# Kernel tuning notes

Hardware: AMD Instinct MI355X
Metric: run time of the kernel (lower is better)

The kernel has to match this reference:

```python
import jax, jax.numpy as jnp
import numpy as np
from jax import lax

B, D, K = 65536, 256, 32  # batch, num_latent_dims, flow_depth


def setup_inputs() -> dict:
    key = jax.random.key(0)
    k1, k2, k3, k4, k5 = jax.random.split(key, 5)
    X = jax.random.normal(k1, (B, D), dtype=jnp.float32)
    h = jax.random.normal(k2, (B, D), dtype=jnp.float32)  # passed through, unused by planar math
    u = jax.random.normal(k3, (K, D), dtype=jnp.float32) * 0.1
    w = jax.random.normal(k4, (K, D), dtype=jnp.float32) * 0.1
    b = jax.random.normal(k5, (K,), dtype=jnp.float32) * 0.1
    return {"X": X, "h": h, "u": u, "w": w, "b": b}


def _planar_chain(z0, u, w, b):
    """Sequential planar normalizing flow: z_{k+1} = z_k + u_hat_k * tanh(w_k.z_k + b_k)."""

    def step(z, params):
        u_k, w_k, b_k = params  # (D,), (D,), scalar
        # enforce invertibility: u_hat so that w.u_hat >= -1
        wu = jnp.dot(w_k, u_k)
        u_hat = u_k + (jax.nn.softplus(wu) - 1.0 - wu) * w_k / jnp.dot(w_k, w_k)
        lin = z @ w_k + b_k              # (B,)
        t = jnp.tanh(lin)                # (B,)
        z_new = z + t[:, None] * u_hat[None, :]
        # psi = (1 - t^2) w ; log|det J| = log|1 + psi.u_hat|
        log_det = jnp.log(jnp.abs(1.0 + (1.0 - t * t) * jnp.dot(w_k, u_hat)) + 1e-8)
        return z_new, log_det

    z_final, log_dets = lax.scan(step, z0, (u, w, b))
    return z_final, log_dets  # (B, D), (K, B)


def reference(X, h, u, w, b):
    z = X.reshape(X.shape[0], X.shape[1])  # view(B, D, -1) then view(B, D) -> (B, D)
    z_final, log_det_jacobians = _planar_chain(z, u, w, b)
    return z_final, log_det_jacobians
```

## Files before the change

kernel.cpp:

```cpp
#include <hip/hip_runtime.h>


typedef __attribute__((ext_vector_type(8))) short short8;
typedef __attribute__((ext_vector_type(4))) float f32x4;

#define B_ 65536
#define D_ 256
#define ROWS 64
#define NTHR 512
#define GRID (B_ / ROWS)

#define WSB_WH 0
#define WSB_WL 16896
#define WSB_UTH 33792
#define WSB_UTL 54272
#define WSB_G 74752
#define WSB_C 78848

#define WH_H 0
#define WL_H 8448
#define UH_H 0
#define UL_H 10240
#define XH_H 20480
#define XL_H 23040
#define LDS_HALVES 25600
#define P_STR 65

__device__ __forceinline__ void bfsplit(float x, unsigned short& h, unsigned short& l) {
  unsigned xb = __float_as_uint(x) & 0xffff0000u;
  h = (unsigned short)(xb >> 16);
  float r = x - __uint_as_float(xb);
  l = (unsigned short)(__float_as_uint(r) >> 16);
}

__global__ __launch_bounds__(256) void nf_gen(const float* __restrict__ u_in,
                                              const float* __restrict__ w_in,
                                              float* __restrict__ ws) {
  __shared__ float wTg[8192];
  __shared__ float ug[8192];
  __shared__ float wu_s[32], ww_s[32], coefs_s[32];
  const int t = threadIdx.x;
  {
    const int k = t & 31, d0 = (t >> 5) * 32;
    const float4* wp = (const float4*)(w_in + k * 256 + d0);
#pragma unroll
    for (int q = 0; q < 8; ++q) {
      float4 v = wp[q];
      wTg[(d0 + q * 4 + 0) * 32 + k] = v.x;
      wTg[(d0 + q * 4 + 1) * 32 + k] = v.y;
      wTg[(d0 + q * 4 + 2) * 32 + k] = v.z;
      wTg[(d0 + q * 4 + 3) * 32 + k] = v.w;
    }
#pragma unroll
    for (int q = 0; q < 8; ++q)
      ((float4*)ug)[t + 256 * q] = ((const float4*)u_in)[t + 256 * q];
  }
  __syncthreads();
  const int k = t & 31, jg = t >> 5;
  float m1[4] = {0.f, 0.f, 0.f, 0.f}, m2[4] = {0.f, 0.f, 0.f, 0.f};
#pragma unroll 4
  for (int dc = 0; dc < 64; ++dc) {
    float wk[4];
    float4 wj[4], uj[4];
#pragma unroll
    for (int i = 0; i < 4; ++i) wk[i] = wTg[(dc * 4 + i) * 32 + k];
#pragma unroll
    for (int i = 0; i < 4; ++i) wj[i] = *(const float4*)&wTg[(dc * 4 + i) * 32 + jg * 4];
#pragma unroll
    for (int i = 0; i < 4; ++i) uj[i] = *(const float4*)&ug[(jg * 4 + i) * 256 + dc * 4];
#pragma unroll
    for (int i = 0; i < 4; ++i) {
      m1[i] = fmaf(uj[i].x, wk[0], m1[i]);
      m1[i] = fmaf(uj[i].y, wk[1], m1[i]);
      m1[i] = fmaf(uj[i].z, wk[2], m1[i]);
      m1[i] = fmaf(uj[i].w, wk[3], m1[i]);
    }
    const float* w0 = (const float*)&wj[0];
    const float* w1 = (const float*)&wj[1];
    const float* w2 = (const float*)&wj[2];
    const float* w3 = (const float*)&wj[3];
#pragma unroll
    for (int i = 0; i < 4; ++i) {
      m2[i] = fmaf(w0[i], wk[0], m2[i]);
      m2[i] = fmaf(w1[i], wk[1], m2[i]);
      m2[i] = fmaf(w2[i], wk[2], m2[i]);
      m2[i] = fmaf(w3[i], wk[3], m2[i]);
    }
  }
  if ((k >> 2) == jg) {
    wu_s[k] = m1[k & 3];
    ww_s[k] = m2[k & 3];
  }
  __syncthreads();
  if (t < 32) {
    float wu = wu_s[t], ww = ww_s[t];
    float sp = fmaxf(wu, 0.f) + log1pf(__expf(-fabsf(wu)));
    coefs_s[t] = (sp - 1.f - wu) / ww;
    ((float*)((char*)ws + WSB_C))[t] = sp - 1.f;
  }
  __syncthreads();
  {
    float* gws = (float*)((char*)ws + WSB_G);
#pragma unroll
    for (int i = 0; i < 4; ++i)
      gws[k * 32 + jg * 4 + i] = fmaf(coefs_s[jg * 4 + i], m2[i], m1[i]);
  }
  {
    const int k2 = t >> 3, d0 = (t & 7) * 32;
    const float ck = coefs_s[k2];
    unsigned short* whp = (unsigned short*)((char*)ws + WSB_WH);
    unsigned short* wlp = (unsigned short*)((char*)ws + WSB_WL);
    unsigned short* uthp = (unsigned short*)((char*)ws + WSB_UTH);
    unsigned short* utlp = (unsigned short*)((char*)ws + WSB_UTL);
    const float4* wp2 = (const float4*)(w_in + k2 * 256 + d0);
    const float4* up2 = (const float4*)(u_in + k2 * 256 + d0);
#pragma unroll
    for (int q = 0; q < 8; ++q) {
      float4 wv = wp2[q], uv = up2[q];
      const float wf[4] = {wv.x, wv.y, wv.z, wv.w};
      const float uf[4] = {uv.x, uv.y, uv.z, uv.w};
#pragma unroll
      for (int i = 0; i < 4; ++i) {
        unsigned short hh, ll;
        bfsplit(wf[i], hh, ll);
        whp[k2 * 264 + d0 + q * 4 + i] = hh;
        wlp[k2 * 264 + d0 + q * 4 + i] = ll;
        float uhv = fmaf(ck, wf[i], uf[i]);
        bfsplit(uhv, hh, ll);
        uthp[(d0 + q * 4 + i) * 40 + k2] = hh;
        utlp[(d0 + q * 4 + i) * 40 + k2] = ll;
      }
    }
  }
}

__global__ __launch_bounds__(NTHR, 6) void nf_fused(const float* __restrict__ X,
                                                    const float* __restrict__ b_in,
                                                    const float* __restrict__ ws,
                                                    float* __restrict__ out) {
  __shared__ __align__(16) unsigned short ldsH[LDS_HALVES];
  float* ldsF = (float*)ldsH;

  const int t = threadIdx.x;
  const int lane = t & 63;
  const int wv = t >> 6;
  const int ln15 = lane & 15;
  const int g = lane >> 4;
  const int g8 = g * 8, g4 = g * 4;
  const int slab = wv >> 1;
  const int nt0 = wv & 1;
  const int row0 = blockIdx.x * ROWS;

  {
    const uint4* wsrc = (const uint4*)((const char*)ws + WSB_WH);
    uint4* wdst = (uint4*)ldsH;
#pragma unroll
    for (int i = 0; i < 4; ++i) wdst[t + 512 * i] = wsrc[t + 512 * i];
    if (t < 64) wdst[2048 + t] = wsrc[2048 + t];
  }

  const int srow = t >> 3;
  const int sd = (t & 7) * 4;
  float4 xr;
  auto load_stage = [&](int cc) {
    xr = *(const float4*)(X + (size_t)(row0 + srow) * 256 + cc * 32 + sd);
  };
  auto store_stage = [&]() {
    const float xf[4] = {xr.x, xr.y, xr.z, xr.w};
    unsigned short h[4], l[4];
#pragma unroll
    for (int e = 0; e < 4; ++e) bfsplit(xf[e], h[e], l[e]);
    *(uint2*)&ldsH[XH_H + srow * 40 + sd] =
        make_uint2((unsigned)h[0] | ((unsigned)h[1] << 16),
                   (unsigned)h[2] | ((unsigned)h[3] << 16));
    *(uint2*)&ldsH[XL_H + srow * 40 + sd] =
        make_uint2((unsigned)l[0] | ((unsigned)l[1] << 16),
                   (unsigned)l[2] | ((unsigned)l[3] << 16));
  };

  f32x4 acc = (f32x4){0.f, 0.f, 0.f, 0.f};
  load_stage(0);
  for (int cc = 0; cc < 8; ++cc) {
    store_stage();
    __syncthreads();
    if (cc < 7) load_stage(cc + 1);
    const int hidx = XH_H + (slab * 16 + ln15) * 40 + g8;
    short8 ah = *(const short8*)&ldsH[hidx];
    short8 al = *(const short8*)&ldsH[hidx + (XL_H - XH_H)];
    const int widx = (nt0 * 16 + ln15) * 264 + cc * 32 + g8;
    short8 bh = *(const short8*)&ldsH[WH_H + widx];
    short8 bl = *(const short8*)&ldsH[WL_H + widx];
    acc = __builtin_amdgcn_mfma_f32_16x16x32_bf16(ah, bh, acc, 0, 0, 0);
    acc = __builtin_amdgcn_mfma_f32_16x16x32_bf16(ah, bl, acc, 0, 0, 0);
    acc = __builtin_amdgcn_mfma_f32_16x16x32_bf16(al, bh, acc, 0, 0, 0);
    __syncthreads();
  }

  {
    const int kcol = nt0 * 16 + ln15;
#pragma unroll
    for (int q = 0; q < 4; ++q)
      ldsF[kcol * P_STR + slab * 16 + g4 + q] = acc[q];
  }
  __syncthreads();

  if (t < 64) {
    const float* gws = (const float*)((const char*)ws + WSB_G);
    const float* cws = (const float*)((const char*)ws + WSB_C);
    float tvv[32];
#pragma unroll
    for (int kk = 0; kk < 32; ++kk) {
      float la = ldsF[kk * P_STR + t] + b_in[kk];
      float lb2 = 0.f;
      const float* gp = gws + kk * 32;
#pragma unroll
      for (int j = 0; j + 1 < kk; j += 2) {
        la = fmaf(tvv[j], gp[j], la);
        lb2 = fmaf(tvv[j + 1], gp[j + 1], lb2);
      }
      if (kk & 1) la = fmaf(tvv[kk - 1], gp[kk - 1], la);
      float lin = la + lb2;
      float e = __expf(2.f * lin);
      float tk = 1.f - 2.f / (e + 1.f);
      tvv[kk] = tk;
      unsigned short hh, ll;
      bfsplit(tk, hh, ll);
      ldsH[XH_H + t * 40 + kk] = hh;
      ldsH[XL_H + t * 40 + kk] = ll;
      float val = fabsf(fmaf(1.f - tk * tk, cws[kk], 1.f)) + 1e-8f;
      out[(size_t)B_ * D_ + (size_t)kk * B_ + row0 + t] = __logf(val);
    }
  }
  __syncthreads();

  {
    const uint4* usrc = (const uint4*)((const char*)ws + WSB_UTH);
    uint4* udst = (uint4*)ldsH;
#pragma unroll
    for (int i = 0; i < 5; ++i) udst[t + 512 * i] = usrc[t + 512 * i];
  }
  __syncthreads();

  {
    const int hidx = XH_H + (slab * 16 + ln15) * 40 + g8;
    short8 tah = *(const short8*)&ldsH[hidx];
    short8 tal = *(const short8*)&ldsH[hidx + (XL_H - XH_H)];
    const size_t rbase = (size_t)row0 + slab * 16 + g4;
#pragma unroll 2
    for (int i = 0; i < 8; ++i) {
      const int nt = nt0 + 2 * i;
      const int uidx = (nt * 16 + ln15) * 40 + g8;
      short8 bh = *(const short8*)&ldsH[UH_H + uidx];
      short8 bl = *(const short8*)&ldsH[UL_H + uidx];
      const int col = nt * 16 + ln15;
      f32x4 c;
#pragma unroll
      for (int q = 0; q < 4; ++q) c[q] = X[(rbase + q) * 256 + col];
      c = __builtin_amdgcn_mfma_f32_16x16x32_bf16(tah, bh, c, 0, 0, 0);
      c = __builtin_amdgcn_mfma_f32_16x16x32_bf16(tah, bl, c, 0, 0, 0);
      c = __builtin_amdgcn_mfma_f32_16x16x32_bf16(tal, bh, c, 0, 0, 0);
#pragma unroll
      for (int q = 0; q < 4; ++q) out[(rbase + q) * 256 + col] = c[q];
    }
  }
}

extern "C" void kernel_launch(void* const* d_in, const int* in_sizes, int n_in,
                              void* d_out, int out_size, void* d_ws, size_t ws_size,
                              hipStream_t stream) {
  const float* X = (const float*)d_in[0];
  const float* u = (const float*)d_in[2];
  const float* w = (const float*)d_in[3];
  const float* b = (const float*)d_in[4];
  float* out = (float*)d_out;
  float* ws = (float*)d_ws;

  nf_gen<<<1, 256, 0, stream>>>(u, w, ws);
  nf_fused<<<GRID, NTHR, 0, stream>>>(X, b, ws, out);
}
```

Baseline: 220.3 us.

## Prefetch all X tiles up front and transpose final MFMA for vector IO

All eight X chunks for the first GEMM are loaded into registers at kernel start, and the X residual tile for the output stage is loaded before the tanh recurrence. The U-hat copy into LDS now also happens before that recurrence, with the partial sums moved to a separate LDS region so the two do not overlap. The final MFMA swaps its operands so each lane owns four consecutive columns, which allows float4 loads of X and float4 stores of the output instead of scalar strided accesses. The cost is more registers and LDS per block, and launch bounds drop from 6 to 4 blocks per CU, which lowers occupancy.

Result: no change. 223.1 us (+1.3%).

```diff
diff --git a/kernel.cpp b/kernel.cpp
--- a/kernel.cpp
+++ b/kernel.cpp
@@ -23,7 +23,8 @@
 #define UL_H 10240
 #define XH_H 20480
 #define XL_H 23040
-#define LDS_HALVES 25600
+#define PF 12800
+#define LDS_HALVES 29760
 #define P_STR 65
 
 __device__ __forceinline__ void bfsplit(float x, unsigned short& h, unsigned short& l) {
@@ -134,7 +135,7 @@
   }
 }
 
-__global__ __launch_bounds__(NTHR, 6) void nf_fused(const float* __restrict__ X,
+__global__ __launch_bounds__(NTHR, 4) void nf_fused(const float* __restrict__ X,
                                                     const float* __restrict__ b_in,
                                                     const float* __restrict__ ws,
                                                     float* __restrict__ out) {
@@ -151,6 +152,13 @@
   const int nt0 = wv & 1;
   const int row0 = blockIdx.x * ROWS;
 
+  const int srow = t >> 3;
+  const int sd = (t & 7) * 4;
+  float4 xp[8];
+#pragma unroll
+  for (int cc = 0; cc < 8; ++cc)
+    xp[cc] = *(const float4*)(X + (size_t)(row0 + srow) * 256 + cc * 32 + sd);
+
   {
     const uint4* wsrc = (const uint4*)((const char*)ws + WSB_WH);
     uint4* wdst = (uint4*)ldsH;
@@ -159,31 +167,22 @@
     if (t < 64) wdst[2048 + t] = wsrc[2048 + t];
   }
 
-  const int srow = t >> 3;
-  const int sd = (t & 7) * 4;
-  float4 xr;
-  auto load_stage = [&](int cc) {
-    xr = *(const float4*)(X + (size_t)(row0 + srow) * 256 + cc * 32 + sd);
-  };
-  auto store_stage = [&]() {
-    const float xf[4] = {xr.x, xr.y, xr.z, xr.w};
-    unsigned short h[4], l[4];
-#pragma unroll
-    for (int e = 0; e < 4; ++e) bfsplit(xf[e], h[e], l[e]);
-    *(uint2*)&ldsH[XH_H + srow * 40 + sd] =
-        make_uint2((unsigned)h[0] | ((unsigned)h[1] << 16),
-                   (unsigned)h[2] | ((unsigned)h[3] << 16));
-    *(uint2*)&ldsH[XL_H + srow * 40 + sd] =
-        make_uint2((unsigned)l[0] | ((unsigned)l[1] << 16),
-                   (unsigned)l[2] | ((unsigned)l[3] << 16));
-  };
-
   f32x4 acc = (f32x4){0.f, 0.f, 0.f, 0.f};
-  load_stage(0);
+#pragma unroll
   for (int cc = 0; cc < 8; ++cc) {
-    store_stage();
+    {
+      const float xf[4] = {xp[cc].x, xp[cc].y, xp[cc].z, xp[cc].w};
+      unsigned short h[4], l[4];
+#pragma unroll
+      for (int e = 0; e < 4; ++e) bfsplit(xf[e], h[e], l[e]);
+      *(uint2*)&ldsH[XH_H + srow * 40 + sd] =
+          make_uint2((unsigned)h[0] | ((unsigned)h[1] << 16),
+                     (unsigned)h[2] | ((unsigned)h[3] << 16));
+      *(uint2*)&ldsH[XL_H + srow * 40 + sd] =
+          make_uint2((unsigned)l[0] | ((unsigned)l[1] << 16),
+                     (unsigned)l[2] | ((unsigned)l[3] << 16));
+    }
     __syncthreads();
-    if (cc < 7) load_stage(cc + 1);
     const int hidx = XH_H + (slab * 16 + ln15) * 40 + g8;
     short8 ah = *(const short8*)&ldsH[hidx];
     short8 al = *(const short8*)&ldsH[hidx + (XL_H - XH_H)];
@@ -200,7 +199,20 @@
     const int kcol = nt0 * 16 + ln15;
 #pragma unroll
     for (int q = 0; q < 4; ++q)
-      ldsF[kcol * P_STR + slab * 16 + g4 + q] = acc[q];
+      ldsF[PF + kcol * P_STR + slab * 16 + g4 + q] = acc[q];
+  }
+  const int prow = slab * 16 + ln15;
+  float4 xc[8];
+#pragma unroll
+  for (int i = 0; i < 8; ++i) {
+    const int nt = nt0 + 2 * i;
+    xc[i] = *(const float4*)(X + (size_t)(row0 + prow) * 256 + nt * 16 + g4);
+  }
+  {
+    const uint4* usrc = (const uint4*)((const char*)ws + WSB_UTH);
+    uint4* udst = (uint4*)ldsH;
+#pragma unroll
+    for (int i = 0; i < 5; ++i) udst[t + 512 * i] = usrc[t + 512 * i];
   }
   __syncthreads();
 
@@ -210,7 +222,7 @@
     float tvv[32];
 #pragma unroll
     for (int kk = 0; kk < 32; ++kk) {
-      float la = ldsF[kk * P_STR + t] + b_in[kk];
+      float la = ldsF[PF + kk * P_STR + t] + b_in[kk];
       float lb2 = 0.f;
       const float* gp = gws + kk * 32;
 #pragma unroll
@@ -234,33 +246,21 @@
   __syncthreads();
 
   {
-    const uint4* usrc = (const uint4*)((const char*)ws + WSB_UTH);
-    uint4* udst = (uint4*)ldsH;
-#pragma unroll
-    for (int i = 0; i < 5; ++i) udst[t + 512 * i] = usrc[t + 512 * i];
-  }
-  __syncthreads();
-
-  {
-    const int hidx = XH_H + (slab * 16 + ln15) * 40 + g8;
-    short8 tah = *(const short8*)&ldsH[hidx];
-    short8 tal = *(const short8*)&ldsH[hidx + (XL_H - XH_H)];
-    const size_t rbase = (size_t)row0 + slab * 16 + g4;
-#pragma unroll 2
+    const int tidx = XH_H + prow * 40 + g8;
+    short8 th = *(const short8*)&ldsH[tidx];
+    short8 tl = *(const short8*)&ldsH[tidx + (XL_H - XH_H)];
+#pragma unroll
     for (int i = 0; i < 8; ++i) {
       const int nt = nt0 + 2 * i;
       const int uidx = (nt * 16 + ln15) * 40 + g8;
-      short8 bh = *(const short8*)&ldsH[UH_H + uidx];
-      short8 bl = *(const short8*)&ldsH[UL_H + uidx];
-      const int col = nt * 16 + ln15;
-      f32x4 c;
-#pragma unroll
-      for (int q = 0; q < 4; ++q) c[q] = X[(rbase + q) * 256 + col];
-      c = __builtin_amdgcn_mfma_f32_16x16x32_bf16(tah, bh, c, 0, 0, 0);
-      c = __builtin_amdgcn_mfma_f32_16x16x32_bf16(tah, bl, c, 0, 0, 0);
-      c = __builtin_amdgcn_mfma_f32_16x16x32_bf16(tal, bh, c, 0, 0, 0);
-#pragma unroll
-      for (int q = 0; q < 4; ++q) out[(rbase + q) * 256 + col] = c[q];
+      short8 uh = *(const short8*)&ldsH[UH_H + uidx];
+      short8 ul = *(const short8*)&ldsH[UL_H + uidx];
+      f32x4 c = {xc[i].x, xc[i].y, xc[i].z, xc[i].w};
+      c = __builtin_amdgcn_mfma_f32_16x16x32_bf16(uh, th, c, 0, 0, 0);
+      c = __builtin_amdgcn_mfma_f32_16x16x32_bf16(uh, tl, c, 0, 0, 0);
+      c = __builtin_amdgcn_mfma_f32_16x16x32_bf16(ul, th, c, 0, 0, 0);
+      *(float4*)(out + (size_t)(row0 + prow) * 256 + nt * 16 + g4) =
+          make_float4(c[0], c[1], c[2], c[3]);
     }
   }
 }
```
